# Kernel optimization log

Measured on AMD Instinct MI355X. Metric: run time of the kernel, lower is better.

The kernel has to match this reference:

```python
import jax, jax.numpy as jnp
import numpy as np

BUCKET_BINS = np.array([0, 1, 2, 3, 4, 5, 7, 8, 15, 16, 31, 32, 63, 64])
SPAN_MAX_LEN = 8  # args.span_maximum_length


def _span_indices(L, W):
    """Enumerate all spans of width 1..min(L,W) over a length-L sequence.
    Matches the torch loop: window w contributes starts 0..L-w, end = start+w.
    Returns static numpy arrays (starts, ends, width-bucket ids)."""
    starts, ends = [], []
    for w in range(1, min(L, W) + 1):
        s = np.arange(0, L - w + 1)
        starts.append(s)
        ends.append(s + w)
    starts = np.concatenate(starts)
    ends = np.concatenate(ends)
    widths = ends - starts
    # bucket_embedding: last index ix with width >= bucket_bins[ix]
    buckets = np.searchsorted(BUCKET_BINS, widths, side='right') - 1
    return starts, ends, buckets


def setup_inputs() -> dict:
    key = jax.random.key(0)
    k1, k2 = jax.random.split(key)
    B, L, D, WDIM = 8, 512, 768, 20
    return {
        "x": jax.random.normal(k1, (B, L, D), dtype=jnp.float32),
        "span_width_emb": jax.random.normal(k2, (len(BUCKET_BINS), WDIM), dtype=jnp.float32),
        "batch_max_seq_len": L,
    }


def reference(x, span_width_emb, batch_max_seq_len):
    # x: [B, L, D]; span enumeration is static given (L, W)
    B = x.shape[0]
    starts, ends, buckets = _span_indices(int(batch_max_seq_len), SPAN_MAX_LEN)
    S = starts.shape[0]
    x_start = x[:, starts, :]            # [B, S, D] gather of start tokens
    x_end = x[:, ends - 1, :]            # [B, S, D] gather of end tokens
    w_emb = span_width_emb[buckets]      # [S, WDIM] width-bucket embedding
    w_emb = jnp.broadcast_to(w_emb[None], (B, S, w_emb.shape[-1]))
    # torch.stack(spans, dim=1) with each span = cat(start, end, width_emb)
    return jnp.concatenate([x_start, x_end, w_emb], axis=-1)  # [B, S, 2D+WDIM]
```

## Files before the change

kernel.cpp:

```cpp
#include <hip/hip_runtime.h>


typedef float f4 __attribute__((ext_vector_type(4)));

#define L_DIM 512
#define S_TOT 4068
#define ROW4  389
#define D4    192

__global__ __launch_bounds__(256) void span_rep_bcast(
    const f4* __restrict__ x,
    const f4* __restrict__ we,
    f4* __restrict__ out)
{
    const int r = blockIdx.x;
    const int b = blockIdx.y;
    const int t = (int)threadIdx.x;

    const int cw[8] = {0, 512, 1023, 1533, 2042, 2550, 3057, 3563};

    const size_t outB = (size_t)b * S_TOT;

    if (t < 192) {
        const f4 v = x[((size_t)b * L_DIM + r) * D4 + t];
        #pragma unroll
        for (int w = 1; w <= 8; ++w) {
            if (r + w <= L_DIM)
                out[(outB + cw[w - 1] + r) * ROW4 + t] = v;
            if (r >= w - 1)
                out[(outB + cw[w - 1] + r - w + 1) * ROW4 + D4 + t] = v;
        }
    } else {
        const int u = t - 192;
        if (u < 40) {
            const int w = u / 5 + 1;
            const int col = u - (w - 1) * 5;
            if (r + w <= L_DIM) {
                const int bucket = (int)((0x765543210ull >> (4 * w)) & 0xF);
                out[(outB + cw[w - 1] + r) * ROW4 + 2 * D4 + col] = we[bucket * 5 + col];
            }
        }
    }
}

extern "C" void kernel_launch(void* const* d_in, const int* in_sizes, int n_in,
                              void* d_out, int out_size, void* d_ws, size_t ws_size,
                              hipStream_t stream) {
    const f4* x  = (const f4*)d_in[0];
    const f4* we = (const f4*)d_in[1];
    f4* out = (f4*)d_out;

    dim3 grid(L_DIM, 8);
    span_rep_bcast<<<grid, 256, 0, stream>>>(x, we, out);
}
```

Before: 209.6 us.

## Switch to output-linear gather with contiguous per-block windows of output rows

```diff
diff --git a/kernel.cpp b/kernel.cpp
--- a/kernel.cpp
+++ b/kernel.cpp
@@ -3,43 +3,48 @@
 
 typedef float f4 __attribute__((ext_vector_type(4)));
 
-#define L_DIM 512
-#define S_TOT 4068
-#define ROW4  389
-#define D4    192
+#define ROW4    389
+#define S_TOT   4068
+#define WIN4    (8 * ROW4)
+#define NBLK    4068
+#define NITER   13
 
-__global__ __launch_bounds__(256) void span_rep_bcast(
+__global__ __launch_bounds__(256) void span_rep_win(
     const f4* __restrict__ x,
     const f4* __restrict__ we,
     f4* __restrict__ out)
 {
-    const int r = blockIdx.x;
-    const int b = blockIdx.y;
-    const int t = (int)threadIdx.x;
+    const int base = blockIdx.x * WIN4;
 
-    const int cw[8] = {0, 512, 1023, 1533, 2042, 2550, 3057, 3563};
+    #pragma unroll
+    for (int i = 0; i < NITER; ++i) {
+        const int local = i * 256 + (int)threadIdx.x;
+        if (i == NITER - 1 && local >= WIN4) continue;
+        const int idx = base + local;
 
-    const size_t outB = (size_t)b * S_TOT;
+        const unsigned row = (unsigned)idx / 389u;
+        const int col = idx - (int)(row * 389u);
+        const unsigned b = row / (unsigned)S_TOT;
+        const int s = (int)row - (int)(b * S_TOT);
 
-    if (t < 192) {
-        const f4 v = x[((size_t)b * L_DIM + r) * D4 + t];
-        #pragma unroll
-        for (int w = 1; w <= 8; ++w) {
-            if (r + w <= L_DIM)
-                out[(outB + cw[w - 1] + r) * ROW4 + t] = v;
-            if (r >= w - 1)
-                out[(outB + cw[w - 1] + r - w + 1) * ROW4 + D4 + t] = v;
-        }
-    } else {
-        const int u = t - 192;
-        if (u < 40) {
-            const int w = u / 5 + 1;
-            const int col = u - (w - 1) * 5;
-            if (r + w <= L_DIM) {
-                const int bucket = (int)((0x765543210ull >> (4 * w)) & 0xF);
-                out[(outB + cw[w - 1] + r) * ROW4 + 2 * D4 + col] = we[bucket * 5 + col];
-            }
-        }
+        int w = 1, cw = 0;
+        if (s >= 512)  { w = 2; cw = 512;  }
+        if (s >= 1023) { w = 3; cw = 1023; }
+        if (s >= 1533) { w = 4; cw = 1533; }
+        if (s >= 2042) { w = 5; cw = 2042; }
+        if (s >= 2550) { w = 6; cw = 2550; }
+        if (s >= 3057) { w = 7; cw = 3057; }
+        if (s >= 3563) { w = 8; cw = 3563; }
+        const int start = s - cw;
+
+        const int r = (col < 192) ? start : (start + w - 1);
+        const int c = (col < 192) ? col : (col - 192);
+        const int xoff = ((int)b * 512 + r) * 192 + c;
+        const int bucket = (int)((0x765543210ull >> (4 * w)) & 0xF);
+        const int woff = bucket * 5 + (col - 384);
+        const f4* src = (col < 384) ? (x + xoff) : (we + woff);
+
+        out[idx] = *src;
     }
 }
 
@@ -50,6 +55,5 @@
     const f4* we = (const f4*)d_in[1];
     f4* out = (f4*)d_out;
 
-    dim3 grid(L_DIM, 8);
-    span_rep_bcast<<<grid, 256, 0, stream>>>(x, we, out);
+    span_rep_win<<<NBLK, 256, 0, stream>>>(x, we, out);
 }
```

New measurement: 210.9 us. About the same (+0.6%).
